# Kernel tuning notes

Measured on AMD Instinct MI355X. Metric: run time of the kernel, lower is better.

Reference implementation:

```python
import jax, jax.numpy as jnp
import numpy as np

N = 8192        # batch_size == num nodes == num hyperedges
D = 512         # hidden_dim
H_HEADS = 8
HD = D // H_HEADS
TOP_K = 16
EPS = 1e-5      # LayerNorm eps


def setup_inputs() -> dict:
    key = jax.random.key(0)
    ks = jax.random.split(key, 10)
    def rn(k, shape, scale=0.02):
        return jax.random.normal(k, shape, dtype=jnp.float32) * scale
    return {
        "x0": jax.random.normal(ks[0], (N, D), dtype=jnp.float32),
        "x1": jax.random.normal(ks[1], (N, D), dtype=jnp.float32),
        # modality projections: Linear -> ReLU -> LayerNorm (per modality)
        "w_p0": rn(ks[2], (D, D)), "b_p0": jnp.zeros((D,), jnp.float32),
        "g0": jnp.ones((D,), jnp.float32), "beta0": jnp.zeros((D,), jnp.float32),
        "w_p1": rn(ks[3], (D, D)), "b_p1": jnp.zeros((D,), jnp.float32),
        "g1": jnp.ones((D,), jnp.float32), "beta1": jnp.zeros((D,), jnp.float32),
        # MultiheadAttention packed in-proj + out-proj
        "in_w": rn(ks[4], (3 * D, D)), "in_b": jnp.zeros((3 * D,), jnp.float32),
        "out_w": rn(ks[5], (D, D)), "out_b": jnp.zeros((D,), jnp.float32),
        # edge weight predictor MLP
        "ew_w1": rn(ks[6], (D // 2, D)), "ew_b1": jnp.zeros((D // 2,), jnp.float32),
        "ew_w2": rn(ks[7], (1, D // 2)), "ew_b2": jnp.zeros((1,), jnp.float32),
    }


def _layernorm(x, g, b):
    m = x.mean(-1, keepdims=True)
    v = ((x - m) ** 2).mean(-1, keepdims=True)
    return (x - m) * jax.lax.rsqrt(v + EPS) * g + b


def _forward(x0, x1, w_p0, b_p0, g0, beta0, w_p1, b_p1, g1, beta1,
             in_w, in_b, out_w, out_b, ew_w1, ew_b1, ew_w2, ew_b2):
    # per-modality projection: Linear -> ReLU -> LayerNorm
    p0 = _layernorm(jax.nn.relu(x0 @ w_p0.T + b_p0), g0, beta0)
    p1 = _layernorm(jax.nn.relu(x1 @ w_p1.T + b_p1), g1, beta1)
    seq = jnp.stack([p0, p1], axis=1)                       # [N, 2, D]
    # cross-modal MHA (self-attention over the 2 modality tokens)
    qkv = seq @ in_w.T + in_b                               # [N, 2, 3D]
    q, k, v = jnp.split(qkv, 3, axis=-1)
    q = q.reshape(N, 2, H_HEADS, HD)
    k = k.reshape(N, 2, H_HEADS, HD)
    v = v.reshape(N, 2, H_HEADS, HD)
    scores = jnp.einsum('bqhd,bkhd->bhqk', q, k) / jnp.sqrt(jnp.float32(HD))
    attn = jax.nn.softmax(scores, axis=-1)                  # [N, h, 2, 2]
    ctx = jnp.einsum('bhqk,bkhd->bqhd', attn, v).reshape(N, 2, D)
    attended = ctx @ out_w.T + out_b                        # [N, 2, D]
    fused = attended.mean(axis=1)                           # [N, D]
    # node-node attention similarity, row-softmax
    sim = jax.nn.softmax(fused @ fused.T, axis=1)           # [N, N]
    _, idx = jax.lax.top_k(sim, TOP_K)                      # [N, K]
    vals = jnp.take_along_axis(sim, idx, axis=1)            # [N, K]
    rows = jnp.arange(N)
    # H[i,i]=1 first, then H[neighbor, i] = sim[i, neighbor] (may overwrite diag)
    H = jnp.zeros((N, N), sim.dtype).at[rows, rows].set(1.0)
    H = H.at[idx, rows[:, None]].set(vals)
    colsum = H.sum(axis=0)
    H = H.at[rows, rows].set(jnp.where(colsum == 0, 1.0, H[rows, rows]))
    # edge weights
    hidden = jax.nn.relu(fused @ ew_w1.T + ew_b1)
    ew = jax.nn.sigmoid(hidden @ ew_w2.T + ew_b2)[:, 0]     # [N]
    ew = jnp.maximum(ew, 1e-8)
    return H, ew


def reference(x0, x1, w_p0, b_p0, g0, beta0, w_p1, b_p1, g1, beta1,
              in_w, in_b, out_w, out_b, ew_w1, ew_b1, ew_w2, ew_b2):
    return _forward(x0, x1, w_p0, b_p0, g0, beta0, w_p1, b_p1, g1, beta1,
                    in_w, in_b, out_w, out_b, ew_w1, ew_b1, ew_w2, ew_b2)
```

## Files before the change

### kernel.cpp

```cpp
#include <hip/hip_runtime.h>
#include <hip/hip_bf16.h>

#define NN 8192
#define DD 512

typedef unsigned short u16;
typedef __bf16 bf16_t;
typedef bf16_t bf16x8 __attribute__((ext_vector_type(8)));
typedef float f32x4 __attribute__((ext_vector_type(4)));

__device__ __forceinline__ float bf2f(u16 h) {
    union { unsigned u; float f; } v; v.u = ((unsigned)h) << 16; return v.f;
}
__device__ __forceinline__ float bflo(unsigned u) {
    union { unsigned u; float f; } v; v.u = u << 16; return v.f;
}
__device__ __forceinline__ float bfhi(unsigned u) {
    union { unsigned u; float f; } v; v.u = u & 0xFFFF0000u; return v.f;
}
__device__ __forceinline__ u16 f2bf(float f) {
    union { float f; unsigned u; } v; v.f = f;
    unsigned r = v.u + 0x7fffu + ((v.u >> 16) & 1u);
    return (u16)(r >> 16);
}

__global__ __launch_bounds__(256) void cvt7(
        const float* __restrict__ s0, u16* __restrict__ d0,
        const float* __restrict__ s1, u16* __restrict__ d1,
        const float* __restrict__ s2, u16* __restrict__ d2,
        const float* __restrict__ s3, u16* __restrict__ d3,
        const float* __restrict__ s4, u16* __restrict__ d4,
        const float* __restrict__ s5, u16* __restrict__ d5,
        const float* __restrict__ s6, u16* __restrict__ d6) {
    size_t v = ((size_t)blockIdx.x * 256 + threadIdx.x) * 8;
    const float* s; u16* d; size_t off;
    if (v < 4194304)      { s = s0; d = d0; off = v; }
    else if (v < 8388608) { s = s1; d = d1; off = v - 4194304; }
    else if (v < 8650752) { s = s2; d = d2; off = v - 8388608; }
    else if (v < 8912896) { s = s3; d = d3; off = v - 8650752; }
    else if (v < 9699328) { s = s4; d = d4; off = v - 8912896; }
    else if (v < 9961472) { s = s5; d = d5; off = v - 9699328; }
    else                  { s = s6; d = d6; off = v - 9961472; }
    float4 a = *(const float4*)(s + off);
    float4 b = *(const float4*)(s + off + 4);
    ushort4 o0 = make_ushort4(f2bf(a.x), f2bf(a.y), f2bf(a.z), f2bf(a.w));
    ushort4 o1 = make_ushort4(f2bf(b.x), f2bf(b.y), f2bf(b.z), f2bf(b.w));
    *(ushort4*)(d + off) = o0;
    *(ushort4*)(d + off + 4) = o1;
}

#define EPS_LDS 136
template<bool RELU, bool BIAS, bool SPLIT>
__global__ __launch_bounds__(256) void gemm_bt(const u16* __restrict__ A,
        const u16* __restrict__ B, const float* __restrict__ bias,
        const u16* __restrict__ B2, const float* __restrict__ bias2, int halfY,
        u16* __restrict__ C, int M, int Nc, int K) {
    __shared__ alignas(16) u16 Smem[2][16384];
    const int t = threadIdx.x;
    const int lane = t & 63;
    const int wave = t >> 6;
    const int wm = (wave >> 1) * 64;
    const int wn = (wave & 1) * 64;
    const int rowA = blockIdx.y * 128;
    const int rowB = blockIdx.x * 128;
    if (SPLIT && (int)blockIdx.y >= halfY) { B = B2; bias = bias2; }

    f32x4 acc[4][4] = {};
    const int mrow = lane & 15;
    const int kk = (lane >> 4) * 8;
    const int nt = K >> 6;

    auto STAGE = [&](int buf, int k0) {
        u16* As = Smem[buf];
        u16* Bs = Smem[buf] + 8192;
        #pragma unroll
        for (int r = 0; r < 4; ++r) {
            int chunk = r * 256 + t;
            const u16* srcA = A + (size_t)(rowA + (chunk >> 3)) * K + k0 + (chunk & 7) * 8;
            __builtin_amdgcn_global_load_lds(
                (const __attribute__((address_space(1))) void*)srcA,
                (__attribute__((address_space(3))) void*)(As + chunk * 8), 16, 0, 0);
            const u16* srcB = B + (size_t)(rowB + (chunk >> 3)) * K + k0 + (chunk & 7) * 8;
            __builtin_amdgcn_global_load_lds(
                (const __attribute__((address_space(1))) void*)srcB,
                (__attribute__((address_space(3))) void*)(Bs + chunk * 8), 16, 0, 0);
        }
    };

    STAGE(0, 0);
    __syncthreads();
    int cur = 0;
    for (int ti = 0; ti < nt; ++ti) {
        if (ti + 1 < nt) STAGE(cur ^ 1, (ti + 1) << 6);
        const u16* As = Smem[cur];
        const u16* Bs = Smem[cur] + 8192;
        #pragma unroll
        for (int ks = 0; ks < 64; ks += 32) {
            bf16x8 af[4], bfv[4];
            #pragma unroll
            for (int i = 0; i < 4; ++i)
                af[i] = *(const bf16x8*)(As + (wm + i * 16 + mrow) * 64 + ks + kk);
            #pragma unroll
            for (int j = 0; j < 4; ++j)
                bfv[j] = *(const bf16x8*)(Bs + (wn + j * 16 + mrow) * 64 + ks + kk);
            #pragma unroll
            for (int i = 0; i < 4; ++i)
                #pragma unroll
                for (int j = 0; j < 4; ++j)
                    acc[i][j] = __builtin_amdgcn_mfma_f32_16x16x32_bf16(af[i], bfv[j], acc[i][j], 0, 0, 0);
        }
        __syncthreads();
        cur ^= 1;
    }

    u16* Ep = &Smem[0][0];
    const int er0 = wm + (lane >> 4) * 4;
    const int ec0 = wn + (lane & 15);
    #pragma unroll
    for (int j = 0; j < 4; ++j) {
        int c = ec0 + j * 16;
        float bv = BIAS ? bias[rowB + c] : 0.0f;
        #pragma unroll
        for (int i = 0; i < 4; ++i) {
            #pragma unroll
            for (int r = 0; r < 4; ++r) {
                float v = acc[i][j][r] + bv;
                if (RELU) v = fmaxf(v, 0.0f);
                Ep[(er0 + i * 16 + r) * EPS_LDS + c] = f2bf(v);
            }
        }
    }
    __syncthreads();
    #pragma unroll
    for (int pass = 0; pass < 8; ++pass) {
        int chunk = pass * 256 + t;
        int rloc = chunk >> 4, coff = (chunk & 15) * 8;
        bf16x8 v = *(const bf16x8*)(Ep + rloc * EPS_LDS + coff);
        *(bf16x8*)(C + (size_t)(rowA + rloc) * Nc + rowB + coff) = v;
    }
}

__global__ __launch_bounds__(256) void gemm_qkv(const u16* __restrict__ A,
        const u16* __restrict__ B, const float* __restrict__ bias,
        u16* __restrict__ V, float* __restrict__ scores) {
    __shared__ alignas(16) u16 Smem[2][16384];
    const int t = threadIdx.x;
    const int lane = t & 63;
    const int wave = t >> 6;
    const int wm = (wave >> 1) * 64;
    const int wn = (wave & 1) * 64;
    const int c = blockIdx.x;
    const int rowA = blockIdx.y * 128;
    const bool isQK = (c < 8);

    f32x4 acc[4][4] = {};
    const int mrow = lane & 15;
    const int kk = (lane >> 4) * 8;

    auto STAGE = [&](int buf, int k0) {
        u16* As = Smem[buf];
        u16* Bs = Smem[buf] + 8192;
        #pragma unroll
        for (int r = 0; r < 4; ++r) {
            int chunk = r * 256 + t;
            int rr = chunk >> 3;
            int brow = isQK ? (c * 64 + rr + ((rr >= 64) ? 448 : 0))
                            : (1024 + (c - 8) * 128 + rr);
            const u16* srcA = A + (size_t)(rowA + rr) * DD + k0 + (chunk & 7) * 8;
            __builtin_amdgcn_global_load_lds(
                (const __attribute__((address_space(1))) void*)srcA,
                (__attribute__((address_space(3))) void*)(As + chunk * 8), 16, 0, 0);
            const u16* srcB = B + (size_t)brow * DD + k0 + (chunk & 7) * 8;
            __builtin_amdgcn_global_load_lds(
                (const __attribute__((address_space(1))) void*)srcB,
                (__attribute__((address_space(3))) void*)(Bs + chunk * 8), 16, 0, 0);
        }
    };

    STAGE(0, 0);
    __syncthreads();
    int cur = 0;
    for (int ti = 0; ti < 8; ++ti) {
        if (ti + 1 < 8) STAGE(cur ^ 1, (ti + 1) << 6);
        const u16* As = Smem[cur];
        const u16* Bs = Smem[cur] + 8192;
        #pragma unroll
        for (int ks = 0; ks < 64; ks += 32) {
            bf16x8 af[4], bfv[4];
            #pragma unroll
            for (int i = 0; i < 4; ++i)
                af[i] = *(const bf16x8*)(As + (wm + i * 16 + mrow) * 64 + ks + kk);
            #pragma unroll
            for (int j = 0; j < 4; ++j)
                bfv[j] = *(const bf16x8*)(Bs + (wn + j * 16 + mrow) * 64 + ks + kk);
            #pragma unroll
            for (int i = 0; i < 4; ++i)
                #pragma unroll
                for (int j = 0; j < 4; ++j)
                    acc[i][j] = __builtin_amdgcn_mfma_f32_16x16x32_bf16(af[i], bfv[j], acc[i][j], 0, 0, 0);
        }
        __syncthreads();
        cur ^= 1;
    }

    u16* Ep = &Smem[0][0];
    const int er0 = wm + (lane >> 4) * 4;
    const int ec0 = wn + (lane & 15);
    #pragma unroll
    for (int j = 0; j < 4; ++j) {
        int cc = ec0 + j * 16;
        int bcol = isQK ? ((cc < 64) ? c * 64 + cc : 448 + c * 64 + cc)
                        : (1024 + (c - 8) * 128 + cc);
        float bv = bias[bcol];
        #pragma unroll
        for (int i = 0; i < 4; ++i) {
            #pragma unroll
            for (int r = 0; r < 4; ++r)
                Ep[(er0 + i * 16 + r) * EPS_LDS + cc] = f2bf(acc[i][j][r] + bv);
        }
    }
    __syncthreads();
    if (isQK) {
        int nd = t >> 2, cb = t & 3, tt2 = cb >> 1, ss = cb & 1;
        const u16* qrow = Ep + (2 * nd + tt2) * EPS_LDS;
        const u16* krow = Ep + (2 * nd + ss) * EPS_LDS + 64;
        float s = 0.0f;
        #pragma unroll
        for (int d8 = 0; d8 < 8; ++d8) {
            bf16x8 qv = *(const bf16x8*)(qrow + d8 * 8);
            bf16x8 kv = *(const bf16x8*)(krow + d8 * 8);
            #pragma unroll
            for (int u = 0; u < 8; ++u) s += (float)qv[u] * (float)kv[u];
        }
        scores[(size_t)(rowA / 2 + nd) * 32 + c * 4 + cb] = s * 0.125f;
    } else {
        #pragma unroll
        for (int pass = 0; pass < 8; ++pass) {
            int chunk = pass * 256 + t;
            int rloc = chunk >> 4, coff = (chunk & 15) * 8;
            bf16x8 v = *(const bf16x8*)(Ep + rloc * EPS_LDS + coff);
            *(bf16x8*)(V + (size_t)(rowA + rloc) * 512 + (c - 8) * 128 + coff) = v;
        }
    }
}

#define SYM_LDS 129
__global__ __launch_bounds__(256) void gemm_symh(const u16* __restrict__ F,
        u16* __restrict__ C, const u16* __restrict__ W1,
        const float* __restrict__ b1, u16* __restrict__ Hid) {
    __shared__ alignas(16) u16 Smem[2][16384];
    const int bx = blockIdx.x, by = blockIdx.y;
    const bool isHid = (bx >= 64);
    if (!isHid && bx < by) return;
    const int t = threadIdx.x;
    const int lane = t & 63;
    const int wave = t >> 6;
    const int wm = (wave >> 1) * 64;
    const int wn = (wave & 1) * 64;
    const int rowI = by * 128;
    const int rowJ = isHid ? (bx - 64) * 128 : bx * 128;
    const u16* Bsrc = isHid ? W1 : F;

    f32x4 acc[4][4] = {};
    const int mrow = lane & 15;
    const int kk = (lane >> 4) * 8;

    auto STAGE = [&](int buf, int k0) {
        u16* As = Smem[buf];
        u16* Bs = Smem[buf] + 8192;
        #pragma unroll
        for (int r = 0; r < 4; ++r) {
            int chunk = r * 256 + t;
            const u16* srcA = F + (size_t)(rowI + (chunk >> 3)) * DD + k0 + (chunk & 7) * 8;
            __builtin_amdgcn_global_load_lds(
                (const __attribute__((address_space(1))) void*)srcA,
                (__attribute__((address_space(3))) void*)(As + chunk * 8), 16, 0, 0);
            const u16* srcB = Bsrc + (size_t)(rowJ + (chunk >> 3)) * DD + k0 + (chunk & 7) * 8;
            __builtin_amdgcn_global_load_lds(
                (const __attribute__((address_space(1))) void*)srcB,
                (__attribute__((address_space(3))) void*)(Bs + chunk * 8), 16, 0, 0);
        }
    };

    STAGE(0, 0);
    __syncthreads();
    int cur = 0;
    for (int ti = 0; ti < 8; ++ti) {
        if (ti + 1 < 8) STAGE(cur ^ 1, (ti + 1) << 6);
        const u16* As = Smem[cur];
        const u16* Bs = Smem[cur] + 8192;
        #pragma unroll
        for (int ks = 0; ks < 64; ks += 32) {
            bf16x8 af[4], bfv[4];
            #pragma unroll
            for (int i = 0; i < 4; ++i)
                af[i] = *(const bf16x8*)(As + (wm + i * 16 + mrow) * 64 + ks + kk);
            #pragma unroll
            for (int j = 0; j < 4; ++j)
                bfv[j] = *(const bf16x8*)(Bs + (wn + j * 16 + mrow) * 64 + ks + kk);
            #pragma unroll
            for (int i = 0; i < 4; ++i)
                #pragma unroll
                for (int j = 0; j < 4; ++j)
                    acc[i][j] = __builtin_amdgcn_mfma_f32_16x16x32_bf16(af[i], bfv[j], acc[i][j], 0, 0, 0);
        }
        __syncthreads();
        cur ^= 1;
    }

    u16* Ep = &Smem[0][0];
    const int er0 = wm + (lane >> 4) * 4;
    const int ec0 = wn + (lane & 15);
    #pragma unroll
    for (int j = 0; j < 4; ++j) {
        int c = ec0 + j * 16;
        float bv = isHid ? b1[rowJ + c] : 0.0f;
        #pragma unroll
        for (int i = 0; i < 4; ++i) {
            #pragma unroll
            for (int r = 0; r < 4; ++r) {
                float v = acc[i][j][r] + bv;
                if (isHid) v = fmaxf(v, 0.0f);
                Ep[(er0 + i * 16 + r) * SYM_LDS + c] = f2bf(v);
            }
        }
    }
    __syncthreads();
    if (isHid) {
        #pragma unroll
        for (int pass = 0; pass < 8; ++pass) {
            int chunk = pass * 256 + t;
            int rloc = chunk >> 4, coff = (chunk & 15) * 8;
            union { u16 us[8]; bf16x8 v; } buf;
            #pragma unroll
            for (int k = 0; k < 8; ++k) buf.us[k] = Ep[rloc * SYM_LDS + coff + k];
            *(bf16x8*)(Hid + (size_t)(rowI + rloc) * 256 + rowJ + coff) = buf.v;
        }
        return;
    }
    #pragma unroll
    for (int pass = 0; pass < 8; ++pass) {
        int chunk = pass * 256 + t;
        int rloc = chunk >> 4, coff = (chunk & 15) * 8;
        union { u16 us[8]; bf16x8 v; } buf;
        #pragma unroll
        for (int k = 0; k < 8; ++k) buf.us[k] = Ep[rloc * SYM_LDS + coff + k];
        *(bf16x8*)(C + (size_t)(rowI + rloc) * NN + rowJ + coff) = buf.v;
    }
    if (bx != by) {
        #pragma unroll
        for (int pass = 0; pass < 8; ++pass) {
            int chunk = pass * 256 + t;
            int tr = chunk >> 4, roff = (chunk & 15) * 8;
            union { u16 us[8]; bf16x8 v; } buf;
            #pragma unroll
            for (int k = 0; k < 8; ++k) buf.us[k] = Ep[(roff + k) * SYM_LDS + tr];
            *(bf16x8*)(C + (size_t)(rowJ + tr) * NN + rowI + roff) = buf.v;
        }
    }
}

__global__ __launch_bounds__(256) void ln2_kernel(const u16* __restrict__ y,
        const float* __restrict__ g0, const float* __restrict__ b0,
        const float* __restrict__ g1, const float* __restrict__ b1,
        u16* __restrict__ seq) {
    int n = blockIdx.x * 4 + (threadIdx.x >> 6);
    int lane = threadIdx.x & 63;
    int modality = n >> 13, node = n & (NN - 1);
    const float* g = modality ? g1 : g0;
    const float* b = modality ? b1 : b0;
    bf16x8 v = *(const bf16x8*)(y + (size_t)n * DD + lane * 8);
    float x[8];
    float s = 0.0f;
    #pragma unroll
    for (int u = 0; u < 8; ++u) { x[u] = (float)v[u]; s += x[u]; }
    #pragma unroll
    for (int off = 32; off; off >>= 1) s += __shfl_xor(s, off);
    float mean = s * (1.0f / DD);
    float vs = 0.0f;
    #pragma unroll
    for (int u = 0; u < 8; ++u) { x[u] -= mean; vs += x[u] * x[u]; }
    #pragma unroll
    for (int off = 32; off; off >>= 1) vs += __shfl_xor(vs, off);
    float inv = rsqrtf(vs * (1.0f / DD) + 1e-5f);
    float4 ga = *(const float4*)(g + lane * 8);
    float4 gb = *(const float4*)(g + lane * 8 + 4);
    float4 ba = *(const float4*)(b + lane * 8);
    float4 bb = *(const float4*)(b + lane * 8 + 4);
    union { u16 us[8]; bf16x8 v; } o;
    o.us[0] = f2bf(x[0] * inv * ga.x + ba.x);
    o.us[1] = f2bf(x[1] * inv * ga.y + ba.y);
    o.us[2] = f2bf(x[2] * inv * ga.z + ba.z);
    o.us[3] = f2bf(x[3] * inv * ga.w + ba.w);
    o.us[4] = f2bf(x[4] * inv * gb.x + bb.x);
    o.us[5] = f2bf(x[5] * inv * gb.y + bb.y);
    o.us[6] = f2bf(x[6] * inv * gb.z + bb.z);
    o.us[7] = f2bf(x[7] * inv * gb.w + bb.w);
    *(bf16x8*)(seq + (size_t)node * (2 * DD) + modality * DD + lane * 8) = o.v;
}

__global__ __launch_bounds__(256) void attn_v(const float* __restrict__ scores,
        const u16* __restrict__ V, u16* __restrict__ ctxm) {
    int n = blockIdx.x * 4 + (threadIdx.x >> 6);
    int lane = threadIdx.x & 63;
    int h = lane >> 3;
    float4 sc = *(const float4*)(scores + (size_t)n * 32 + h * 4);
    float s00 = sc.x, s01 = sc.y, s10 = sc.z, s11 = sc.w;
    float m0 = fmaxf(s00, s01), e00 = __expf(s00 - m0), e01 = __expf(s01 - m0);
    float a00 = e00 / (e00 + e01), a01 = e01 / (e00 + e01);
    float m1 = fmaxf(s10, s11), e10 = __expf(s10 - m1), e11 = __expf(s11 - m1);
    float a10 = e10 / (e10 + e11), a11 = e11 / (e10 + e11);
    float al0 = 0.5f * (a00 + a10), al1 = 0.5f * (a01 + a11);
    bf16x8 v0 = *(const bf16x8*)(V + (size_t)(2 * n) * 512 + lane * 8);
    bf16x8 v1 = *(const bf16x8*)(V + (size_t)(2 * n + 1) * 512 + lane * 8);
    union { u16 us[8]; bf16x8 v; } o;
    #pragma unroll
    for (int u = 0; u < 8; ++u)
        o.us[u] = f2bf(al0 * (float)v0[u] + al1 * (float)v1[u]);
    *(bf16x8*)(ctxm + (size_t)n * 512 + lane * 8) = o.v;
}

__global__ __launch_bounds__(256) void topk_bf16(const u16* __restrict__ S,
        float* __restrict__ topv, int* __restrict__ topi,
        const u16* __restrict__ hidden, const float* __restrict__ w2,
        const float* __restrict__ b2, float* __restrict__ ew_out) {
    const int blk = blockIdx.x;
    const int t = threadIdx.x;
    if (blk >= 2048) {
        int wv = t >> 6, lane = t & 63;
        int n0 = (blk - 2048) * 64 + wv * 16;
        float wa = w2[lane], wb = w2[lane + 64], wc = w2[lane + 128], wd = w2[lane + 192];
        for (int q = 0; q < 16; ++q) {
            int n = n0 + q;
            const u16* hr = hidden + (size_t)n * 256;
            float s = bf2f(hr[lane]) * wa + bf2f(hr[lane + 64]) * wb
                    + bf2f(hr[lane + 128]) * wc + bf2f(hr[lane + 192]) * wd;
            #pragma unroll
            for (int off = 32; off; off >>= 1) s += __shfl_xor(s, off);
            if (lane == 0) {
                float z = s + b2[0];
                float sig = 1.0f / (1.0f + __expf(-z));
                ew_out[n] = fmaxf(sig, 1e-8f);
            }
        }
        return;
    }
    const float NEG = -3e38f;
    int row = blk * 4 + (t >> 6);
    int lane = t & 63;
    const u16* Sr = S + (size_t)row * NN;

    float m = NEG, l = 0.0f;
    float t1v = NEG, t2v = NEG;
    int t1i = 0x7FFFFFFF, t2i = 0x7FFFFFFF;

    #pragma unroll
    for (int p = 0; p < 16; ++p) {
        uint4 raw = *(const uint4*)(Sr + p * 512 + lane * 8);
        int base = p * 512 + lane * 8;
        #pragma unroll
        for (int q = 0; q < 4; ++q) {
            unsigned w = (&raw.x)[q];
            #pragma unroll
            for (int h = 0; h < 2; ++h) {
                float x = h ? bfhi(w) : bflo(w);
                int xi = base + q * 2 + h;
                if (x > m) { l = l * __expf(m - x) + 1.0f; m = x; }
                else l += __expf(x - m);
                bool g1 = x > t1v, g2 = x > t2v;
                t2v = g1 ? t1v : (g2 ? x : t2v);
                t2i = g1 ? t1i : (g2 ? xi : t2i);
                t1v = g1 ? x : t1v;
                t1i = g1 ? xi : t1i;
            }
        }
    }
    #pragma unroll
    for (int off = 32; off; off >>= 1) {
        float om = __shfl_xor(m, off);
        float ol = __shfl_xor(l, off);
        float nm = fmaxf(m, om);
        l = l * __expf(m - nm) + ol * __expf(om - nm);
        m = nm;
    }

    unsigned mk0 = 0, mk1 = 0, mk2 = 0, mk3 = 0;
    float cv = t1v; int ci = t1i;
    float bv = t2v; int bi = t2i;
    for (int r = 0; r < 16; ++r) {
        float wv = cv; int wi = ci;
        #pragma unroll
        for (int off = 32; off; off >>= 1) {
            float ov = __shfl_xor(wv, off);
            int oi = __shfl_xor(wi, off);
            if (ov > wv || (ov == wv && oi < wi)) { wv = ov; wi = oi; }
        }
        if (lane == 0) {
            topv[(size_t)row * 16 + r] = __expf(wv - m) / l;
            topi[(size_t)row * 16 + r] = wi;
        }
        if (wi == ci) {
            int slot = ((wi >> 9) << 3) | (wi & 7);
            unsigned bit = 1u << (slot & 31);
            if (slot < 32) mk0 |= bit; else if (slot < 64) mk1 |= bit;
            else if (slot < 96) mk2 |= bit; else mk3 |= bit;
            cv = bv; ci = bi;
            bv = NEG; bi = 0x7FFFFFFF;
            if (ci == 0x7FFFFFFF) {
                float nb = NEG; int ni = 0x7FFFFFFF;
                #pragma unroll
                for (int p = 0; p < 16; ++p) {
                    uint4 raw = *(const uint4*)(Sr + p * 512 + lane * 8);
                    int base = p * 512 + lane * 8;
                    #pragma unroll
                    for (int q = 0; q < 4; ++q) {
                        unsigned w = (&raw.x)[q];
                        #pragma unroll
                        for (int h = 0; h < 2; ++h) {
                            int sl = p * 8 + q * 2 + h;
                            unsigned mw = (sl < 32) ? mk0 : (sl < 64) ? mk1
                                        : (sl < 96) ? mk2 : mk3;
                            float x = ((mw >> (sl & 31)) & 1u) ? NEG
                                    : (h ? bfhi(w) : bflo(w));
                            if (x > nb) { nb = x; ni = base + q * 2 + h; }
                        }
                    }
                }
                cv = nb; ci = ni;
            }
        }
    }
}

__global__ __launch_bounds__(256) void scatter_diag(const float* __restrict__ topv,
        const int* __restrict__ topi, float* __restrict__ H) {
    int tk = blockIdx.x * 256 + threadIdx.x;
    if (tk < NN * 16) {
        int i = tk >> 4;
        int idx = topi[tk];
        H[(size_t)idx * NN + i] = topv[tk];
    } else {
        int c = tk - NN * 16;
        const int* ti = topi + c * 16;
        bool self = false;
        #pragma unroll
        for (int j = 0; j < 16; ++j) self |= (ti[j] == c);
        if (!self) H[(size_t)c * NN + c] = 1.0f;
    }
}

extern "C" void kernel_launch(void* const* d_in, const int* in_sizes, int n_in,
                              void* d_out, int out_size, void* d_ws, size_t ws_size,
                              hipStream_t stream) {
    const float* x0    = (const float*)d_in[0];
    const float* x1    = (const float*)d_in[1];
    const float* w_p0  = (const float*)d_in[2];
    const float* b_p0  = (const float*)d_in[3];
    const float* g0    = (const float*)d_in[4];
    const float* beta0 = (const float*)d_in[5];
    const float* w_p1  = (const float*)d_in[6];
    const float* b_p1  = (const float*)d_in[7];
    const float* g1    = (const float*)d_in[8];
    const float* beta1 = (const float*)d_in[9];
    const float* in_w  = (const float*)d_in[10];
    const float* in_b  = (const float*)d_in[11];
    const float* out_w = (const float*)d_in[12];
    const float* out_b = (const float*)d_in[13];
    const float* ew_w1 = (const float*)d_in[14];
    const float* ew_b1 = (const float*)d_in[15];
    const float* ew_w2 = (const float*)d_in[16];
    const float* ew_b2 = (const float*)d_in[17];

    float* Hf = (float*)d_out;
    float* ew_out = Hf + (size_t)NN * NN;

    u16* Hu = (u16*)d_out;
    u16* x0b    = Hu;
    u16* x1b    = Hu + 4194304;
    u16* y01    = Hu + 8388608;
    u16* seq    = Hu + 16777216;
    u16* Vbuf   = Hu + 25165824;
    u16* ctxm   = Hu + 50331648;
    u16* hidden = Hu + 54525952;
    float* scB  = (float*)(Hu + 58720256);
    u16* wp0b   = Hu + 60817408;
    u16* wp1b   = wp0b + 262144;
    u16* inwb   = wp1b + 262144;
    u16* outwb  = inwb + 786432;
    u16* eww1b  = outwb + 262144;
    u16* Sb     = Hu + 67108864;
    char* ws = (char*)d_ws;
    u16* fusedB = (u16*)ws;
    float* topv = (float*)(ws + (8u << 20));
    int*   topi = (int*)(ws + (8u << 20) + 524288);

    dim3 blk(256);
    const int BIG = 1 << 30;
    cvt7<<<dim3(4928), blk, 0, stream>>>(x0, x0b, x1, x1b, w_p0, wp0b, w_p1, wp1b,
                                         in_w, inwb, out_w, outwb, ew_w1, eww1b);
    gemm_bt<true, true, true><<<dim3(4, 128), blk, 0, stream>>>(
        x0b, wp0b, b_p0, wp1b, b_p1, 64, y01, 2 * NN, DD, DD);
    ln2_kernel<<<dim3(2 * NN / 4), blk, 0, stream>>>(y01, g0, beta0, g1, beta1, seq);
    gemm_qkv<<<dim3(12, 128), blk, 0, stream>>>(seq, inwb, in_b, Vbuf, scB);
    attn_v<<<dim3(NN / 4), blk, 0, stream>>>(scB, Vbuf, ctxm);
    gemm_bt<false, true, false><<<dim3(4, 64), blk, 0, stream>>>(
        ctxm, outwb, out_b, nullptr, nullptr, BIG, fusedB, NN, DD, DD);
    gemm_symh<<<dim3(66, 64), blk, 0, stream>>>(fusedB, Sb, eww1b, ew_b1, hidden);
    topk_bf16<<<dim3(2176), blk, 0, stream>>>(Sb, topv, topi,
        hidden, ew_w2, ew_b2, ew_out);
    hipMemsetAsync(Hf, 0, (size_t)NN * NN * sizeof(float), stream);
    scatter_diag<<<dim3((NN * 16 + NN) / 256), blk, 0, stream>>>(topv, topi, Hf);
}
```

Before: 624.3 us.

## Fuse H zero-fill into top-k kernel and track three candidates per lane

Drops the separate full-matrix hipMemsetAsync of H. The top-k kernel now zeroes its share of H itself, skipping the sub-regions that alias the similarity matrix and hidden buffers. Each block also zeroes its own S rows and hidden rows once it has consumed them, so the whole aliased buffer ends up zero. The idea is to overlap the large zero-fill writes with the top-k compute instead of paying for them as a separate bandwidth-bound pass. The per-lane candidate list also grows from two to three entries, so the costly masked rescan of a row happens less often, at the cost of a few more registers and selects in the main loop. This relies on hard-coded byte offsets for the workspace aliasing, which is fragile.

```diff
diff --git a/kernel.cpp b/kernel.cpp
--- a/kernel.cpp
+++ b/kernel.cpp
@@ -420,12 +420,14 @@
     *(bf16x8*)(ctxm + (size_t)n * 512 + lane * 8) = o.v;
 }
 
-__global__ __launch_bounds__(256) void topk_bf16(const u16* __restrict__ S,
+__global__ __launch_bounds__(256) void topk_bf16(u16* __restrict__ S,
         float* __restrict__ topv, int* __restrict__ topi,
-        const u16* __restrict__ hidden, const float* __restrict__ w2,
-        const float* __restrict__ b2, float* __restrict__ ew_out) {
+        u16* __restrict__ hidden, const float* __restrict__ w2,
+        const float* __restrict__ b2, float* __restrict__ ew_out,
+        float* __restrict__ H) {
     const int blk = blockIdx.x;
     const int t = threadIdx.x;
+    const float4 z4 = make_float4(0.f, 0.f, 0.f, 0.f);
     if (blk >= 2048) {
         int wv = t >> 6, lane = t & 63;
         int n0 = (blk - 2048) * 64 + wv * 16;
@@ -443,16 +445,20 @@
                 ew_out[n] = fmaxf(sig, 1e-8f);
             }
         }
+        float4* zb = (float4*)(hidden + (size_t)n0 * 256);
+        #pragma unroll
+        for (int i = 0; i < 8; ++i) zb[i * 64 + lane] = z4;
         return;
     }
     const float NEG = -3e38f;
+    const int SENT = 0x7FFFFFFF;
     int row = blk * 4 + (t >> 6);
     int lane = t & 63;
-    const u16* Sr = S + (size_t)row * NN;
+    u16* Sr = S + (size_t)row * NN;
 
     float m = NEG, l = 0.0f;
-    float t1v = NEG, t2v = NEG;
-    int t1i = 0x7FFFFFFF, t2i = 0x7FFFFFFF;
+    float t1v = NEG, t2v = NEG, t3v = NEG;
+    int t1i = SENT, t2i = SENT, t3i = SENT;
 
     #pragma unroll
     for (int p = 0; p < 16; ++p) {
@@ -467,7 +473,9 @@
                 int xi = base + q * 2 + h;
                 if (x > m) { l = l * __expf(m - x) + 1.0f; m = x; }
                 else l += __expf(x - m);
-                bool g1 = x > t1v, g2 = x > t2v;
+                bool g1 = x > t1v, g2 = x > t2v, g3 = x > t3v;
+                t3v = g2 ? t2v : (g3 ? x : t3v);
+                t3i = g2 ? t2i : (g3 ? xi : t3i);
                 t2v = g1 ? t1v : (g2 ? x : t2v);
                 t2i = g1 ? t1i : (g2 ? xi : t2i);
                 t1v = g1 ? x : t1v;
@@ -485,10 +493,10 @@
     }
 
     unsigned mk0 = 0, mk1 = 0, mk2 = 0, mk3 = 0;
-    float cv = t1v; int ci = t1i;
-    float bv = t2v; int bi = t2i;
+    float c1v = t1v, c2v = t2v, c3v = t3v;
+    int c1i = t1i, c2i = t2i, c3i = t3i;
     for (int r = 0; r < 16; ++r) {
-        float wv = cv; int wi = ci;
+        float wv = c1v; int wi = c1i;
         #pragma unroll
         for (int off = 32; off; off >>= 1) {
             float ov = __shfl_xor(wv, off);
@@ -499,15 +507,16 @@
             topv[(size_t)row * 16 + r] = __expf(wv - m) / l;
             topi[(size_t)row * 16 + r] = wi;
         }
-        if (wi == ci) {
+        if (wi == c1i) {
             int slot = ((wi >> 9) << 3) | (wi & 7);
             unsigned bit = 1u << (slot & 31);
             if (slot < 32) mk0 |= bit; else if (slot < 64) mk1 |= bit;
             else if (slot < 96) mk2 |= bit; else mk3 |= bit;
-            cv = bv; ci = bi;
-            bv = NEG; bi = 0x7FFFFFFF;
-            if (ci == 0x7FFFFFFF) {
-                float nb = NEG; int ni = 0x7FFFFFFF;
+            c1v = c2v; c1i = c2i;
+            c2v = c3v; c2i = c3i;
+            c3v = NEG; c3i = SENT;
+            if (c1i == SENT) {
+                float nb = NEG; int ni = SENT;
                 #pragma unroll
                 for (int p = 0; p < 16; ++p) {
                     uint4 raw = *(const uint4*)(Sr + p * 512 + lane * 8);
@@ -526,7 +535,24 @@
                         }
                     }
                 }
-                cv = nb; ci = ni;
+                c1v = nb; c1i = ni;
+            }
+        }
+    }
+
+    float4* srow = (float4*)Sr;
+    #pragma unroll
+    for (int i = 0; i < 16; ++i) srow[i * 64 + lane] = z4;
+
+    {
+        size_t vb0 = (size_t)blk * 63488;
+        #pragma unroll
+        for (int rr = 0; rr < 16; ++rr) {
+            int j = rr * 256 + t;
+            if (j < 3968) {
+                size_t b = vb0 + (size_t)j * 16;
+                char* p = (char*)H + (b < 109051904u ? b : b + 4194304u);
+                *(float4*)p = z4;
             }
         }
     }
@@ -607,7 +633,6 @@
         ctxm, outwb, out_b, nullptr, nullptr, BIG, fusedB, NN, DD, DD);
     gemm_symh<<<dim3(66, 64), blk, 0, stream>>>(fusedB, Sb, eww1b, ew_b1, hidden);
     topk_bf16<<<dim3(2176), blk, 0, stream>>>(Sb, topv, topi,
-        hidden, ew_w2, ew_b2, ew_out);
-    hipMemsetAsync(Hf, 0, (size_t)NN * NN * sizeof(float), stream);
+        hidden, ew_w2, ew_b2, ew_out, Hf);
     scatter_diag<<<dim3((NN * 16 + NN) / 256), blk, 0, stream>>>(topv, topi, Hf);
 }
```

New measurement: 570.4 us. 8.6% less time.
